# Optimization experiments

Hardware: AMD Instinct MI355X
Metric: run time of the kernel (lower is better)

The kernel has to match this reference:

```python
import jax, jax.numpy as jnp
import numpy as np

N, E, B, H, F = 20000, 400000, 200, 10, 78
HID = H * F  # 780
SEQ, VOC, EMB, NF, KS = 1000, 26, 128, 32, 8
CONV_OUT = SEQ - KS + 1  # 993


def setup_inputs() -> dict:
    key = jax.random.key(0)
    ks = jax.random.split(key, 40)
    g = lambda i, shape, s=0.05: jax.random.normal(ks[i], shape, jnp.float32) * s
    inp = {
        "x": jax.random.normal(ks[0], (N, F), jnp.float32),
        "edge_index": jax.random.randint(ks[1], (2, E), 0, N),
        "batch": jnp.sort(jax.random.randint(ks[2], (N,), 0, B)),
        "target": jax.random.randint(ks[3], (B, SEQ), 0, VOC),
        # GATConv(78 -> 78, heads=10)
        "gat_W": g(4, (F, HID)),
        "gat_a_src": g(5, (H, F)),
        "gat_a_dst": g(6, (H, F)),
        "gat_b": g(7, (HID,)),
        # GCNConv(780 -> 780)
        "gcn_W": g(8, (HID, HID)),
        "gcn_b": g(9, (HID,)),
        # graph MLP head
        "fcg1_W": g(10, (HID, 1500)), "fcg1_b": g(11, (1500,)),
        "fcg2_W": g(12, (1500, 128)), "fcg2_b": g(13, (128,)),
        # protein branch
        "emb": g(14, (VOC, EMB)),
        "cW": g(15, (NF, EMB, KS)), "cb": g(16, (NF,)),
        "fxt_W": g(17, (NF * CONV_OUT, 128)), "fxt_b": g(18, (128,)),
        # fusion MLP
        "f1_W": g(19, (256, 1024)), "f1_b": g(20, (1024,)),
        "f2_W": g(21, (1024, 512)), "f2_b": g(22, (512,)),
        "f3_W": g(23, (512, 256)), "f3_b": g(24, (256,)),
        "f4_W": g(25, (256, 128)), "f4_b": g(26, (128,)),
        "o_W": g(27, (128, 1)), "o_b": g(28, (1,)),
    }
    return inp


def _graph_branch(x, edge_index, batch, gat_W, gat_a_src, gat_a_dst, gat_b,
                  gcn_W, gcn_b, fcg1_W, fcg1_b, fcg2_W, fcg2_b):
    n = x.shape[0]
    loops = jnp.arange(n)
    src = jnp.concatenate([edge_index[0], loops])  # add self loops (PyG default)
    dst = jnp.concatenate([edge_index[1], loops])
    # --- GATConv ---
    h = (x @ gat_W).reshape(n, H, F)  # [N,H,F]
    a_s = jnp.einsum("nhf,hf->nh", h, gat_a_src)
    a_d = jnp.einsum("nhf,hf->nh", h, gat_a_dst)
    e = jax.nn.leaky_relu(a_s[src] + a_d[dst], 0.2)  # [Etot,H]
    m = jax.ops.segment_max(e, dst, num_segments=n)
    ex = jnp.exp(e - m[dst])
    den = jax.ops.segment_sum(ex, dst, num_segments=n)
    alpha = ex / den[dst]
    agg = jax.ops.segment_sum(h[src] * alpha[:, :, None], dst, num_segments=n)
    x1 = jax.nn.relu(agg.reshape(n, HID) + gat_b)
    # --- GCNConv (sym norm with self loops) ---
    deg = jax.ops.segment_sum(jnp.ones_like(dst, jnp.float32), dst, num_segments=n)
    dinv = jax.lax.rsqrt(jnp.maximum(deg, 1.0))
    norm = dinv[src] * dinv[dst]
    h2 = x1 @ gcn_W
    x2 = jax.ops.segment_sum(h2[src] * norm[:, None], dst, num_segments=n) + gcn_b
    x2 = jax.nn.relu(x2)
    # --- global add pool + MLP ---
    xg = jax.ops.segment_sum(x2, batch, num_segments=B)
    xg = jax.nn.relu(xg @ fcg1_W + fcg1_b)  # dropout = identity (eval)
    return xg @ fcg2_W + fcg2_b


def _protein_branch(target, emb, cW, cb, fxt_W, fxt_b):
    et = emb[target]  # [B,SEQ,EMB]
    c = jax.lax.conv_general_dilated(
        et.transpose(0, 2, 1), cW, (1,), "VALID",
        dimension_numbers=("NCH", "OIH", "NCH"))  # [B,NF,993]
    c = c + cb[None, :, None]
    return c.reshape(c.shape[0], NF * CONV_OUT) @ fxt_W + fxt_b


def reference(x, edge_index, batch, target, gat_W, gat_a_src, gat_a_dst, gat_b,
              gcn_W, gcn_b, fcg1_W, fcg1_b, fcg2_W, fcg2_b, emb, cW, cb,
              fxt_W, fxt_b, f1_W, f1_b, f2_W, f2_b, f3_W, f3_b, f4_W, f4_b,
              o_W, o_b):
    xg = _graph_branch(x, edge_index, batch, gat_W, gat_a_src, gat_a_dst, gat_b,
                       gcn_W, gcn_b, fcg1_W, fcg1_b, fcg2_W, fcg2_b)
    xt = _protein_branch(target, emb, cW, cb, fxt_W, fxt_b)
    xc = jnp.concatenate([xg, xt], axis=1)  # [B,256]
    xc = jax.nn.relu(xc @ f1_W + f1_b)
    xc = jax.nn.relu(xc @ f2_W + f2_b)
    xc = jax.nn.relu(xc @ f3_W + f3_b)
    xc = jax.nn.relu(xc @ f4_W + f4_b)
    return xc @ o_W + o_b  # [B,1]
```

## Files before the change

kernel.cpp:

```cpp
#include <hip/hip_runtime.h>
#include <hip/hip_bf16.h>
#include <math.h>

typedef __hip_bfloat16 bf16;
typedef __attribute__((ext_vector_type(8))) short short8v;
typedef __attribute__((ext_vector_type(4))) float float4v;

#define NODES 20000
#define EDG   400000
#define ETOT  (EDG + NODES)
#define GB    200
#define HEADS 10
#define FD    78
#define HIDD  780
#define SEQL  1000
#define VOCS  26
#define EMBD  128
#define NFC   32
#define KSZ   8
#define COUT  993
#define KFXT  (NFC * COUT)

#define MPAD  20096
#define NPADB 896
#define KP1   96
#define KP2   800
#define HP    800
#define PNL   4
#define PF    200


__device__ __forceinline__ float us2f(unsigned short u) {
  unsigned int i = ((unsigned int)u) << 16; float f; __builtin_memcpy(&f, &i, 4); return f;
}
__device__ __forceinline__ float b2f(bf16 v) { return __bfloat162float(v); }
__device__ __forceinline__ float ldany(const void* p, size_t i, int m) {
  if (m) return ((const float*)p)[i];
  return b2f(((const bf16*)p)[i]);
}
__device__ __forceinline__ bool nanf_(float v) { return v != v; }
__device__ __forceinline__ unsigned short f2us(float v) {
  bf16 b = __float2bfloat16(v); unsigned short u; __builtin_memcpy(&u, &b, 2); return u;
}

__global__ void k_detect(const void* x, int* diag) {
  int t = threadIdx.x;
  const unsigned short* u = (const unsigned short*)x;
  int hit = 0;
  for (int i = t; i < 4096; i += 256) {
    float v = us2f(u[i]);
    if (nanf_(v) || fabsf(v) > 1e6f) hit = 1;
  }
  if (hit) diag[1] = 1;
}

__global__ void k_pad_x(const void* x, bf16* xpad, const int* diag) {
  int idx = blockIdx.x * 256 + threadIdx.x;
  if (idx >= MPAD * KP1) return;
  int mode = diag[1];
  int m = idx / KP1, k = idx % KP1;
  float v = (m < NODES && k < FD) ? ldany(x, (size_t)m * FD + k, mode) : 0.f;
  xpad[idx] = __float2bfloat16(v);
}

__global__ void k_tr_gatw(const void* gw, bf16* Wt, const int* diag) {
  int idx = blockIdx.x * 256 + threadIdx.x;
  if (idx >= NPADB * KP1) return;
  int mode = diag[1];
  int n = idx / KP1, k = idx % KP1;
  float v = (n < HIDD && k < FD) ? ldany(gw, (size_t)k * HIDD + n, mode) : 0.f;
  Wt[idx] = __float2bfloat16(v);
}

__global__ void k_tr_gcnw(const void* gw, bf16* Wt, const int* diag) {
  int idx = blockIdx.x * 256 + threadIdx.x;
  if (idx >= NPADB * KP2) return;
  int mode = diag[1];
  int n = idx / KP2, k = idx % KP2;
  float v = (n < HIDD && k < HIDD) ? ldany(gw, (size_t)k * HIDD + n, mode) : 0.f;
  Wt[idx] = __float2bfloat16(v);
}

__global__ void k_zero_x1pad(bf16* x1p) {
  int i = blockIdx.x * 256 + threadIdx.x;
  if (i < (MPAD - NODES) * KP2)
    x1p[(size_t)NODES * KP2 + i] = __float2bfloat16(0.f);
}

#define MT 128
#define NT 128
#define BK 32
#define LP 40
__global__ __launch_bounds__(256) void k_gemm_mfma(const bf16* A, int lda,
                                                   const bf16* Bt, int ldb,
                                                   bf16* C, int ldc, int Ncap,
                                                   int M, int Kp) {
  __shared__ __align__(16) bf16 As[MT * LP];
  __shared__ __align__(16) bf16 Bs[NT * LP];
  int t = threadIdx.x;
  int lane = t & 63, w = t >> 6;
  int wr = (w >> 1) * 64, wc = (w & 1) * 64;
  int quad = lane >> 4, mr = lane & 15;
  int m0 = blockIdx.y * MT, n0 = blockIdx.x * NT;
  float4v acc[4][4];
#pragma unroll
  for (int i = 0; i < 4; ++i)
#pragma unroll
    for (int j = 0; j < 4; ++j) acc[i][j] = (float4v){0.f, 0.f, 0.f, 0.f};

  for (int kc = 0; kc < Kp; kc += BK) {
#pragma unroll
    for (int i = 0; i < 4; ++i) {
      int c = t + i * 256;
      int row = c >> 3, col = (c & 7) * 4;
      *(uint2*)&As[row * LP + col] =
          *(const uint2*)&A[(size_t)(m0 + row) * lda + kc + col];
      *(uint2*)&Bs[row * LP + col] =
          *(const uint2*)&Bt[(size_t)(n0 + row) * ldb + kc + col];
    }
    __syncthreads();
    short8v af[4], bfr[4];
#pragma unroll
    for (int i = 0; i < 4; ++i)
      af[i] = *(const short8v*)&As[(wr + i * 16 + mr) * LP + quad * 8];
#pragma unroll
    for (int j = 0; j < 4; ++j)
      bfr[j] = *(const short8v*)&Bs[(wc + j * 16 + mr) * LP + quad * 8];
#pragma unroll
    for (int i = 0; i < 4; ++i)
#pragma unroll
      for (int j = 0; j < 4; ++j)
        acc[i][j] = __builtin_amdgcn_mfma_f32_16x16x32_bf16(af[i], bfr[j], acc[i][j], 0, 0, 0);
    __syncthreads();
  }
#pragma unroll
  for (int i = 0; i < 4; ++i) {
    int gm0 = m0 + wr + i * 16 + quad * 4;
#pragma unroll
    for (int j = 0; j < 4; ++j) {
      int gn = n0 + wc + j * 16 + mr;
      if (gn >= Ncap) continue;
#pragma unroll
      for (int r = 0; r < 4; ++r) {
        int gm = gm0 + r;
        if (gm < M) C[(size_t)gm * ldc + gn] = __float2bfloat16(acc[i][j][r]);
      }
    }
  }
}

#define MLP_NT 64
#define MLP_BK 32
#define MLP_MT 208
#define MLP_LP 40
__global__ __launch_bounds__(256) void k_mlp_mfma(const void* A, int lda, const void* Bw,
                                                  const void* bias, float* out, int ostride,
                                                  int ooff, int M, int Nn, int K,
                                                  int ksplit, int aRelu, int aBf16,
                                                  const int* diag) {
  __shared__ __align__(16) bf16 As[MLP_MT * MLP_LP];
  __shared__ __align__(16) bf16 Bs[MLP_NT * MLP_LP];
  int mode = diag[1];
  int t = threadIdx.x;
  int lane = t & 63, w = t >> 6;
  int quad = lane >> 4, mr = lane & 15;
  int n0 = blockIdx.x * MLP_NT;
  int kz = blockIdx.y;
  int nchunks = (K + MLP_BK - 1) / MLP_BK;
  int cpk = (nchunks + ksplit - 1) / ksplit;
  int c0 = kz * cpk, c1 = c0 + cpk;
  if (c1 > nchunks) c1 = nchunks;
  float4v acc[13];
#pragma unroll
  for (int i = 0; i < 13; ++i) acc[i] = (float4v){0.f, 0.f, 0.f, 0.f};

  for (int c = c0; c < c1; ++c) {
    int k0 = c * MLP_BK;
    if (aBf16) {
      const bf16* Ab = (const bf16*)A;
      for (int e = t; e < MLP_MT * 4; e += 256) {
        int row = e >> 2, c8 = (e & 3) * 8;
        int gk = k0 + c8;
        if (row < M && gk + 7 < K) {
          *(uint4*)&As[row * MLP_LP + c8] = *(const uint4*)&Ab[(size_t)row * lda + gk];
        } else {
#pragma unroll
          for (int kk = 0; kk < 8; ++kk) {
            float v = (row < M && gk + kk < K) ? b2f(Ab[(size_t)row * lda + gk + kk]) : 0.f;
            As[row * MLP_LP + c8 + kk] = __float2bfloat16(v);
          }
        }
      }
    } else {
      const float* Af = (const float*)A;
      for (int e = t; e < MLP_MT * 8; e += 256) {
        int row = e >> 3, c4 = (e & 7) * 4;
        int gk = k0 + c4;
        float4 v4 = {0.f, 0.f, 0.f, 0.f};
        if (row < M) {
          if (gk + 3 < K) {
            v4 = *(const float4*)&Af[(size_t)row * lda + gk];
          } else {
            v4.x = (gk + 0 < K) ? Af[(size_t)row * lda + gk + 0] : 0.f;
            v4.y = (gk + 1 < K) ? Af[(size_t)row * lda + gk + 1] : 0.f;
            v4.z = (gk + 2 < K) ? Af[(size_t)row * lda + gk + 2] : 0.f;
            v4.w = (gk + 3 < K) ? Af[(size_t)row * lda + gk + 3] : 0.f;
          }
        }
        if (aRelu) {
          v4.x = fmaxf(v4.x, 0.f); v4.y = fmaxf(v4.y, 0.f);
          v4.z = fmaxf(v4.z, 0.f); v4.w = fmaxf(v4.w, 0.f);
        }
        bf16* dst = &As[row * MLP_LP + c4];
        dst[0] = __float2bfloat16(v4.x); dst[1] = __float2bfloat16(v4.y);
        dst[2] = __float2bfloat16(v4.z); dst[3] = __float2bfloat16(v4.w);
      }
    }
    for (int e = t; e < MLP_NT * MLP_BK; e += 256) {
      int k = e >> 6, col = e & 63;
      int gk = k0 + k, gn = n0 + col;
      float v = (gn < Nn && gk < K) ? ldany(Bw, (size_t)gk * Nn + gn, mode) : 0.f;
      Bs[col * MLP_LP + k] = __float2bfloat16(v);
    }
    __syncthreads();
    short8v bf = *(const short8v*)&Bs[(w * 16 + mr) * MLP_LP + quad * 8];
#pragma unroll
    for (int i = 0; i < 13; ++i) {
      short8v af = *(const short8v*)&As[(i * 16 + mr) * MLP_LP + quad * 8];
      acc[i] = __builtin_amdgcn_mfma_f32_16x16x32_bf16(af, bf, acc[i], 0, 0, 0);
    }
    __syncthreads();
  }
  int gn = n0 + w * 16 + mr;
  if (gn >= Nn) return;
  float bs = (kz == 0) ? ldany(bias, gn, mode) : 0.f;
#pragma unroll
  for (int i = 0; i < 13; ++i) {
    int gm0 = i * 16 + quad * 4;
#pragma unroll
    for (int r = 0; r < 4; ++r) {
      int gm = gm0 + r;
      if (gm >= M) break;
      float v = acc[i][r] + bs;
      float* op = &out[(size_t)gm * ostride + ooff + gn];
      if (ksplit == 1) *op = v;
      else atomicAdd(op, v);
    }
  }
}

__global__ void k_prep_ws(const void* gat_W, const void* a_src, const void* a_dst,
                          float* Ws, float* Wd, const int* diag) {
  int idx = blockIdx.x * 256 + threadIdx.x;
  if (idx >= FD * HEADS) return;
  int mode = diag[1];
  int k = idx / HEADS, hd = idx % HEADS;
  float s = 0.f, d = 0.f;
  for (int f = 0; f < FD; ++f) {
    float w = ldany(gat_W, (size_t)k * HIDD + hd * FD + f, mode);
    s += w * ldany(a_src, (size_t)hd * FD + f, mode);
    d += w * ldany(a_dst, (size_t)hd * FD + f, mode);
  }
  Ws[k * HEADS + hd] = s;
  Wd[k * HEADS + hd] = d;
}

__global__ void k_prep_mtab(const void* emb, const void* cW, float* Mtab, const int* diag) {
  int idx = blockIdx.x * 256 + threadIdx.x;
  if (idx >= NFC * KSZ * VOCS) return;
  int mode = diag[1];
  int o = idx / (KSZ * VOCS);
  int r = idx % (KSZ * VOCS);
  int k = r / VOCS, v = r % VOCS;
  float acc = 0.f;
  for (int i = 0; i < EMBD; ++i)
    acc += ldany(emb, (size_t)v * EMBD + i, mode) * ldany(cW, ((size_t)o * EMBD + i) * KSZ + k, mode);
  Mtab[idx] = acc;
}

__global__ __launch_bounds__(256) void k_asd(const void* x, const float* Ws, const float* Wd,
                                             float* a_s, float* a_d, const int* diag) {
  __shared__ unsigned short xs[256 * FD];
  __shared__ float ws_sh[FD * HEADS], wd_sh[FD * HEADS];
  int mode = diag[1];
  int nb = blockIdx.x * 256, t = threadIdx.x;
  for (int e = t; e < FD * HEADS; e += 256) { ws_sh[e] = Ws[e]; wd_sh[e] = Wd[e]; }
  for (int e = t; e < 256 * FD; e += 256) {
    int r = e / FD, c = e % FD;
    int gn = nb + r;
    float xv = (gn < NODES) ? ldany(x, (size_t)gn * FD + c, mode) : 0.f;
    xs[e] = f2us(xv);
  }
  __syncthreads();
  int n = nb + t;
  if (n >= NODES) return;
  float as[HEADS], ad[HEADS];
#pragma unroll
  for (int hd = 0; hd < HEADS; ++hd) { as[hd] = 0.f; ad[hd] = 0.f; }
  for (int f = 0; f < FD; ++f) {
    float xv = us2f(xs[t * FD + f]);
#pragma unroll
    for (int hd = 0; hd < HEADS; ++hd) {
      as[hd] += xv * ws_sh[f * HEADS + hd];
      ad[hd] += xv * wd_sh[f * HEADS + hd];
    }
  }
#pragma unroll
  for (int hd = 0; hd < HEADS; ++hd) {
    a_s[n * HEADS + hd] = as[hd];
    a_d[n * HEADS + hd] = ad[hd];
  }
}

__global__ void k_count(const int* ei, int* cnt, int* diag) {
  int e = blockIdx.x * 256 + threadIdx.x;
  if (e >= ETOT) return;
  int d = (e < EDG) ? ei[EDG + e] : (e - EDG);
  if ((unsigned)d >= NODES) { atomicOr(diag, 8192); d = 0; }
  atomicAdd(&cnt[d], 1);
}

__global__ __launch_bounds__(1024) void k_scan(const int* cnt, int* rowstart) {
  __shared__ int sh[1024];
  __shared__ int carry;
  int t = threadIdx.x;
  if (t == 0) carry = 0;
  __syncthreads();
  for (int c = 0; c < (NODES + 1023) / 1024; ++c) {
    int i = c * 1024 + t;
    int v = (i < NODES) ? cnt[i] : 0;
    sh[t] = v;
    __syncthreads();
    for (int off = 1; off < 1024; off <<= 1) {
      int add = (t >= off) ? sh[t - off] : 0;
      __syncthreads();
      sh[t] += add;
      __syncthreads();
    }
    int tot = sh[1023];
    int excl = sh[t] - v + carry;
    if (i < NODES) rowstart[i] = excl;
    __syncthreads();
    if (t == 0) carry += tot;
    __syncthreads();
  }
  if (t == 0) rowstart[NODES] = carry;
}

__global__ void k_dinv(const int* cnt, float* dinv) {
  int n = blockIdx.x * 256 + threadIdx.x;
  if (n >= NODES) return;
  int d = cnt[n];
  dinv[n] = rsqrtf((float)(d > 0 ? d : 1));
}

__global__ void k_scatter(const int* ei, const int* rowstart, int* cur, int* es_src,
                          int* diag) {
  int e = blockIdx.x * 256 + threadIdx.x;
  if (e >= ETOT) return;
  int s, d;
  if (e < EDG) { s = ei[e]; d = ei[EDG + e]; } else { s = e - EDG; d = s; }
  if ((unsigned)d >= NODES) { atomicOr(diag, 8192); d = 0; }
  if ((unsigned)s >= NODES) { atomicOr(diag, 8192); s = 0; }
  int pos = rowstart[d] + atomicAdd(&cur[d], 1);
  if ((unsigned)pos < (unsigned)ETOT) es_src[pos] = s;
  else atomicOr(diag, 1);
}

__global__ void k_csrchk(const int* cnt, const int* cur, const int* rowst, int* diag) {
  int n = blockIdx.x * 256 + threadIdx.x;
  if (n < NODES && cur[n] != cnt[n]) atomicOr(diag, 1);
  if (n == 0 && rowst[NODES] != ETOT) atomicOr(diag, 1);
}

__global__ void k_bseg(const int* batch, int* bstart, int* diag) {
  int i = blockIdx.x * 256 + threadIdx.x;
  if (i >= NODES) return;
  int bi = batch[i];
  if ((unsigned)bi >= GB) { atomicOr(diag, 8192); bi = GB - 1; }
  int bp;
  if (i == 0) bp = -1;
  else {
    bp = batch[i - 1];
    if ((unsigned)bp >= GB) bp = GB - 1;
  }
  for (int b = bp + 1; b <= bi; ++b) bstart[b] = i;
  if (i == NODES - 1)
    for (int b = bi + 1; b <= GB; ++b) bstart[b] = NODES;
}

__global__ __launch_bounds__(64) void k_alpha(const int* es_src, const int* rowst,
                                              const float* a_s, const float* a_d,
                                              float* alpha, int* diag) {
  int d = blockIdx.x, lane = threadIdx.x;
  int start = rowst[d], end = rowst[d + 1];
  float ad[HEADS];
#pragma unroll
  for (int j = 0; j < HEADS; ++j) ad[j] = a_d[d * HEADS + j];
  float mx[HEADS];
#pragma unroll
  for (int j = 0; j < HEADS; ++j) mx[j] = -INFINITY;
  for (int base = start; base < end; base += 64) {
    int ce = base + lane;
    if (ce < end) {
      int s = es_src[ce];
      if ((unsigned)s >= NODES) { atomicOr(diag, 1); s = 0; }
#pragma unroll
      for (int j = 0; j < HEADS; ++j) {
        float v = a_s[s * HEADS + j] + ad[j];
        v = v > 0.f ? v : 0.2f * v;
        mx[j] = fmaxf(mx[j], v);
      }
    }
  }
#pragma unroll
  for (int j = 0; j < HEADS; ++j)
    for (int off = 1; off < 64; off <<= 1) mx[j] = fmaxf(mx[j], __shfl_xor(mx[j], off, 64));
  float den[HEADS];
#pragma unroll
  for (int j = 0; j < HEADS; ++j) den[j] = 0.f;
  for (int base = start; base < end; base += 64) {
    int ce = base + lane;
    if (ce < end) {
      int s = es_src[ce];
      if ((unsigned)s >= NODES) s = 0;
#pragma unroll
      for (int j = 0; j < HEADS; ++j) {
        float v = a_s[s * HEADS + j] + ad[j];
        v = v > 0.f ? v : 0.2f * v;
        den[j] += expf(v - mx[j]);
      }
    }
  }
#pragma unroll
  for (int j = 0; j < HEADS; ++j)
    for (int off = 1; off < 64; off <<= 1) den[j] += __shfl_xor(den[j], off, 64);
  if (lane == 0 && (nanf_(den[0]) || nanf_(den[HEADS - 1]))) atomicOr(diag, 2);
  for (int base = start; base < end; base += 64) {
    int ce = base + lane;
    if (ce < end) {
      int s = es_src[ce];
      if ((unsigned)s >= NODES) s = 0;
#pragma unroll
      for (int j = 0; j < HEADS; ++j) {
        float v = a_s[s * HEADS + j] + ad[j];
        v = v > 0.f ? v : 0.2f * v;
        alpha[(size_t)ce * HEADS + j] = expf(v - mx[j]) / den[j];
      }
    }
  }
}

__global__ __launch_bounds__(64) void k_gatg(const int* es_src, const int* rowst,
                                             const float* alpha, const bf16* h,
                                             const void* gat_b, bf16* x1, int* diag) {
  __shared__ int ssc[64];
  __shared__ float alw[64 * HEADS];
  int bid = blockIdx.x;
  int p = bid & (PNL - 1), d = bid >> 2;
  int lane = threadIdx.x;
  int mode = diag[1];
  int start = rowst[d], end = rowst[d + 1];
  int fb = p * PF + lane * 4;
  int hA = fb / FD; if (hA > HEADS - 1) hA = HEADS - 1;
  int hB = (fb + 3) / FD; if (hB > HEADS - 1) hB = HEADS - 1;
  bool selB[4];
#pragma unroll
  for (int k = 0; k < 4; ++k) {
    int hk = (fb + k) / FD; if (hk > HEADS - 1) hk = HEADS - 1;
    selB[k] = (hk != hA);
  }
  float acc[4] = {0.f, 0.f, 0.f, 0.f};
  for (int base = start; base < end; base += 64) {
    int ce = base + lane;
    if (ce < end) {
      int s = es_src[ce];
      if ((unsigned)s >= NODES) { atomicOr(diag, 1); s = 0; }
      ssc[lane] = s;
#pragma unroll
      for (int j = 0; j < HEADS; ++j) alw[lane * HEADS + j] = alpha[(size_t)ce * HEADS + j];
    }
    __syncthreads();
    int cnt2 = end - base; if (cnt2 > 64) cnt2 = 64;
    if (lane < 50) {
      for (int e = 0; e < cnt2; ++e) {
        int ss = ssc[e];
        float aA = alw[e * HEADS + hA];
        float aB = alw[e * HEADS + hB];
        uint2 u = *(const uint2*)(h + (size_t)ss * HP + fb);
        acc[0] += (selB[0] ? aB : aA) * us2f((unsigned short)(u.x & 0xffffu));
        acc[1] += (selB[1] ? aB : aA) * us2f((unsigned short)(u.x >> 16));
        acc[2] += (selB[2] ? aB : aA) * us2f((unsigned short)(u.y & 0xffffu));
        acc[3] += (selB[3] ? aB : aA) * us2f((unsigned short)(u.y >> 16));
      }
    }
    __syncthreads();
  }
  if (lane < 50) {
    if (nanf_(acc[0]) || nanf_(acc[3])) atomicOr(diag, 8);
    unsigned short o[4];
#pragma unroll
    for (int k = 0; k < 4; ++k) {
      int f = fb + k;
      float v = 0.f;
      if (f < HIDD) v = fmaxf(acc[k] + ldany(gat_b, f, mode), 0.f);
      o[k] = f2us(v);
    }
    uint2 pack;
    __builtin_memcpy(&pack, o, 8);
    *(uint2*)(x1 + (size_t)d * KP2 + fb) = pack;
  }
}

__global__ __launch_bounds__(64) void k_gcng(const int* es_src, const int* rowst,
                                             const float* dinv, const bf16* h2,
                                             const void* gcn_b, bf16* x2b, int* diag) {
  __shared__ int ssc[64];
  __shared__ float nw[64];
  int bid = blockIdx.x;
  int p = bid & (PNL - 1), d = bid >> 2;
  int lane = threadIdx.x;
  int mode = diag[1];
  int start = rowst[d], end = rowst[d + 1];
  float dd = dinv[d];
  int fb = p * PF + lane * 4;
  float acc[4] = {0.f, 0.f, 0.f, 0.f};
  for (int base = start; base < end; base += 64) {
    int ce = base + lane;
    if (ce < end) {
      int s = es_src[ce];
      if ((unsigned)s >= NODES) { atomicOr(diag, 1); s = 0; }
      ssc[lane] = s;
      nw[lane] = dinv[s] * dd;
    }
    __syncthreads();
    int cnt2 = end - base; if (cnt2 > 64) cnt2 = 64;
    if (lane < 50) {
      for (int e = 0; e < cnt2; ++e) {
        int ss = ssc[e];
        float nv = nw[e];
        uint2 u = *(const uint2*)(h2 + (size_t)ss * HP + fb);
        acc[0] += nv * us2f((unsigned short)(u.x & 0xffffu));
        acc[1] += nv * us2f((unsigned short)(u.x >> 16));
        acc[2] += nv * us2f((unsigned short)(u.y & 0xffffu));
        acc[3] += nv * us2f((unsigned short)(u.y >> 16));
      }
    }
    __syncthreads();
  }
  if (lane < 50) {
    if (nanf_(acc[0]) || nanf_(acc[3])) atomicOr(diag, 16);
    unsigned short o[4];
#pragma unroll
    for (int k = 0; k < 4; ++k) {
      int f = fb + k;
      float v = 0.f;
      if (f < HIDD) v = fmaxf(acc[k] + ldany(gcn_b, f, mode), 0.f);
      o[k] = f2us(v);
    }
    uint2 pack;
    __builtin_memcpy(&pack, o, 8);
    *(uint2*)(x2b + (size_t)d * HP + fb) = pack;
  }
}

__global__ __launch_bounds__(256) void k_pool(const bf16* x2b, const int* bstart,
                                              float* xg_pool) {
  int b = blockIdx.x, t = threadIdx.x;
  if (t >= 195) return;
  int r0 = bstart[b], r1 = bstart[b + 1];
  int fb = t * 4;
  float4 acc = {0.f, 0.f, 0.f, 0.f};
  for (int r = r0; r < r1; ++r) {
    uint2 u = *(const uint2*)(x2b + (size_t)r * HP + fb);
    acc.x += us2f((unsigned short)(u.x & 0xffffu));
    acc.y += us2f((unsigned short)(u.x >> 16));
    acc.z += us2f((unsigned short)(u.y & 0xffffu));
    acc.w += us2f((unsigned short)(u.y >> 16));
  }
  *(float4*)&xg_pool[(size_t)b * HIDD + fb] = acc;
}

__global__ __launch_bounds__(256) void k_conv(const int* target, const float* Mtab,
                                              const void* cb, bf16* c, int* diag) {
  int b = blockIdx.y, tc = blockIdx.x, t = threadIdx.x;
  __shared__ float Mt[NFC * KSZ * VOCS];
  __shared__ int tg[256 + KSZ - 1];
  int mode = diag[1];
  for (int e = t; e < NFC * KSZ * VOCS; e += 256) Mt[e] = Mtab[e];
  int tbase = tc * 256;
  for (int e = t; e < 256 + KSZ - 1; e += 256) {
    int p = tbase + e;
    int tv = (p < SEQL) ? target[b * SEQL + p] : 0;
    if ((unsigned)tv >= VOCS) { atomicOr(diag, 8192); tv = 0; }
    tg[e] = tv;
  }
  __syncthreads();
  int tt = tbase + t;
  if (tt >= COUT) return;
  float acc[NFC];
#pragma unroll
  for (int o = 0; o < NFC; ++o) acc[o] = 0.f;
#pragma unroll
  for (int k = 0; k < KSZ; ++k) {
    int v = tg[t + k];
    const float* Mk = &Mt[k * VOCS + v];
#pragma unroll
    for (int o = 0; o < NFC; ++o) acc[o] += Mk[o * KSZ * VOCS];
  }
  if (nanf_(acc[0])) atomicOr(diag, 4096);
#pragma unroll
  for (int o = 0; o < NFC; ++o)
    c[(size_t)b * KFXT + o * COUT + tt] = __float2bfloat16(acc[o] + ldany(cb, o, mode));
}

__global__ __launch_bounds__(64) void k_out(const float* xf4, const void* o_W,
                                            const void* o_b, void* outp, const int* diag) {
  int b = blockIdx.x, lane = threadIdx.x;
  int mode = diag[1];
  float a0 = fmaxf(xf4[b * 128 + lane], 0.f);
  float a1 = fmaxf(xf4[b * 128 + 64 + lane], 0.f);
  float v = a0 * ldany(o_W, lane, mode) + a1 * ldany(o_W, 64 + lane, mode);
  for (int off = 32; off; off >>= 1) v += __shfl_down(v, off, 64);
  if (lane == 0) {
    float r = v + ldany(o_b, 0, mode);
    int dg = diag[0];
    if (dg) r = 256.f * (1 + mode) + 8.f * (float)(__ffs(dg) - 1);
    else if (nanf_(r)) r = 200.f + 100.f * mode;
    if (mode) ((float*)outp)[b] = r;
    else ((bf16*)outp)[b] = __float2bfloat16(r);
  }
}

extern "C" void kernel_launch(void* const* d_in, const int* in_sizes, int n_in,
                              void* d_out, int out_size, void* d_ws, size_t ws_size,
                              hipStream_t stream) {
  const void* x       = d_in[0];
  const int*  ei      = (const int*)d_in[1];
  const int*  batch   = (const int*)d_in[2];
  const int*  target  = (const int*)d_in[3];
  const void* gat_W   = d_in[4];
  const void* a_src   = d_in[5];
  const void* a_dst   = d_in[6];
  const void* gat_b   = d_in[7];
  const void* gcn_W   = d_in[8];
  const void* gcn_b   = d_in[9];
  const void* fcg1_W  = d_in[10];
  const void* fcg1_b  = d_in[11];
  const void* fcg2_W  = d_in[12];
  const void* fcg2_b  = d_in[13];
  const void* emb     = d_in[14];
  const void* cW      = d_in[15];
  const void* cb      = d_in[16];
  const void* fxt_W   = d_in[17];
  const void* fxt_b   = d_in[18];
  const void* f1_W    = d_in[19];
  const void* f1_b    = d_in[20];
  const void* f2_W    = d_in[21];
  const void* f2_b    = d_in[22];
  const void* f3_W    = d_in[23];
  const void* f3_b    = d_in[24];
  const void* f4_W    = d_in[25];
  const void* f4_b    = d_in[26];
  const void* o_W     = d_in[27];
  const void* o_b     = d_in[28];

  char* w = (char*)d_ws;
  size_t off = 0;
  auto alloc = [&](size_t bytes) -> void* {
    void* p = w + off;
    off = (off + bytes + 255) & ~(size_t)255;
    return p;
  };
  bf16*  h_buf   = (bf16*)alloc((size_t)NODES * HP * 2);
  bf16*  x1p     = (bf16*)alloc((size_t)MPAD * KP2 * 2);
  bf16*  xpad    = (bf16*)alloc((size_t)MPAD * KP1 * 2);
  bf16*  gatWt   = (bf16*)alloc((size_t)NPADB * KP1 * 2);
  bf16*  gcnWt   = (bf16*)alloc((size_t)NPADB * KP2 * 2);
  float* a_s     = (float*)alloc((size_t)NODES * HEADS * 4);
  float* a_d     = (float*)alloc((size_t)NODES * HEADS * 4);
  float* alpha   = (float*)alloc((size_t)ETOT * HEADS * 4);
  float* Ws      = (float*)alloc(FD * HEADS * 4);
  float* Wd      = (float*)alloc(FD * HEADS * 4);
  float* Mtab    = (float*)alloc(NFC * KSZ * VOCS * 4);
  int*   rowst   = (int*)alloc((NODES + 1) * 4);
  float* dinv    = (float*)alloc(NODES * 4);
  int*   bstart  = (int*)alloc((GB + 1) * 4);
  bf16*  c_buf   = (bf16*)alloc((size_t)GB * KFXT * 2);
  size_t zoff = off;
  int*   cnt     = (int*)alloc(NODES * 4);
  int*   cur     = (int*)alloc(NODES * 4);
  int*   es_src  = (int*)alloc((size_t)ETOT * 4);
  float* xg_pool = (float*)alloc((size_t)GB * HIDD * 4);
  float* xg1     = (float*)alloc((size_t)GB * 1500 * 4);
  float* xc      = (float*)alloc((size_t)GB * 256 * 4);
  float* xf1     = (float*)alloc((size_t)GB * 1024 * 4);
  float* xf2     = (float*)alloc((size_t)GB * 512 * 4);
  float* xf3     = (float*)alloc((size_t)GB * 256 * 4);
  float* xf4     = (float*)alloc((size_t)GB * 128 * 4);
  int*   diag    = (int*)alloc(2 * 4);
  size_t zlen = off - zoff;

  bf16* x2b = x1p;

  hipMemsetAsync(w + zoff, 0, zlen, stream);

  k_detect<<<1, 256, 0, stream>>>(x, diag);

  k_pad_x<<<(MPAD * KP1 + 255) / 256, 256, 0, stream>>>(x, xpad, diag);
  k_tr_gatw<<<(NPADB * KP1 + 255) / 256, 256, 0, stream>>>(gat_W, gatWt, diag);
  k_tr_gcnw<<<(NPADB * KP2 + 255) / 256, 256, 0, stream>>>(gcn_W, gcnWt, diag);
  k_zero_x1pad<<<((MPAD - NODES) * KP2 + 255) / 256, 256, 0, stream>>>(x1p);

  k_prep_ws<<<(FD * HEADS + 255) / 256, 256, 0, stream>>>(gat_W, a_src, a_dst, Ws, Wd, diag);
  k_prep_mtab<<<(NFC * KSZ * VOCS + 255) / 256, 256, 0, stream>>>(emb, cW, Mtab, diag);

  k_gemm_mfma<<<dim3(NPADB / NT, MPAD / MT), 256, 0, stream>>>(
      xpad, KP1, gatWt, KP1, h_buf, HP, HP, NODES, KP1);
  k_asd<<<(NODES + 255) / 256, 256, 0, stream>>>(x, Ws, Wd, a_s, a_d, diag);

  k_count<<<(ETOT + 255) / 256, 256, 0, stream>>>(ei, cnt, diag);
  k_scan<<<1, 1024, 0, stream>>>(cnt, rowst);
  k_dinv<<<(NODES + 255) / 256, 256, 0, stream>>>(cnt, dinv);
  k_scatter<<<(ETOT + 255) / 256, 256, 0, stream>>>(ei, rowst, cur, es_src, diag);
  k_csrchk<<<(NODES + 255) / 256, 256, 0, stream>>>(cnt, cur, rowst, diag);
  k_bseg<<<(NODES + 255) / 256, 256, 0, stream>>>(batch, bstart, diag);

  k_alpha<<<NODES, 64, 0, stream>>>(es_src, rowst, a_s, a_d, alpha, diag);
  k_gatg<<<NODES * PNL, 64, 0, stream>>>(es_src, rowst, alpha, h_buf, gat_b, x1p, diag);

  k_gemm_mfma<<<dim3(NPADB / NT, MPAD / MT), 256, 0, stream>>>(
      x1p, KP2, gcnWt, KP2, h_buf, HP, HP, NODES, KP2);

  k_gcng<<<NODES * PNL, 64, 0, stream>>>(es_src, rowst, dinv, h_buf, gcn_b, x2b, diag);
  k_pool<<<GB, 256, 0, stream>>>(x2b, bstart, xg_pool);

  k_conv<<<dim3(4, GB), 256, 0, stream>>>(target, Mtab, cb, c_buf, diag);

  k_mlp_mfma<<<dim3(24, 4), 256, 0, stream>>>(xg_pool, HIDD, fcg1_W, fcg1_b,
                                              xg1, 1500, 0, GB, 1500, HIDD, 4, 0, 0, diag);
  k_mlp_mfma<<<dim3(2, 16), 256, 0, stream>>>(xg1, 1500, fcg2_W, fcg2_b,
                                              xc, 256, 0, GB, 128, 1500, 16, 1, 0, diag);
  k_mlp_mfma<<<dim3(2, 64), 256, 0, stream>>>(c_buf, KFXT, fxt_W, fxt_b,
                                              xc, 256, 128, GB, 128, KFXT, 64, 0, 1, diag);
  k_mlp_mfma<<<dim3(16, 4), 256, 0, stream>>>(xc, 256, f1_W, f1_b,
                                              xf1, 1024, 0, GB, 1024, 256, 4, 0, 0, diag);
  k_mlp_mfma<<<dim3(8, 8), 256, 0, stream>>>(xf1, 1024, f2_W, f2_b,
                                             xf2, 512, 0, GB, 512, 1024, 8, 1, 0, diag);
  k_mlp_mfma<<<dim3(4, 8), 256, 0, stream>>>(xf2, 512, f3_W, f3_b,
                                             xf3, 256, 0, GB, 256, 512, 8, 1, 0, diag);
  k_mlp_mfma<<<dim3(2, 8), 256, 0, stream>>>(xf3, 256, f4_W, f4_b,
                                             xf4, 128, 0, GB, 128, 256, 8, 1, 0, diag);
  k_out<<<GB, 64, 0, stream>>>(xf4, o_W, o_b, d_out, diag);
}
```

Before: 958.6 us.

## Transpose conv output and split fxt GEMM over 128 K-slices with reduction

The protein conv now writes its output transposed ([K, batch padded to 208]), one block per filter and 32-position tile. A dedicated fxt GEMM kernel splits the 31776-long K dimension into 128 slices, writes partial sums to a scratch buffer instead of using atomics, and a separate kernel reduces them and adds the bias. The aim is more parallelism for the large-K, small-M GEMM and removal of atomic contention on xc. The cost is an extra partial buffer of 128x208x128 floats, an extra launch, and uncoalesced transposed scatter stores into the A tile in shared memory.

```diff
diff --git a/kernel.cpp b/kernel.cpp
--- a/kernel.cpp
+++ b/kernel.cpp
@@ -28,6 +28,8 @@
 #define HP    800
 #define PNL   4
 #define PF    200
+#define MB2   208
+#define FXT_KS 128
 
 
 __device__ __forceinline__ float us2f(unsigned short u) {
@@ -249,6 +251,71 @@
   }
 }
 
+__global__ __launch_bounds__(256) void k_fxt(const bf16* cT, const void* Bw,
+                                             float* part, const int* diag) {
+  __shared__ __align__(16) bf16 As[MLP_MT * MLP_LP];
+  __shared__ __align__(16) bf16 Bs[MLP_NT * MLP_LP];
+  int mode = diag[1];
+  int t = threadIdx.x;
+  int lane = t & 63, w = t >> 6;
+  int quad = lane >> 4, mr = lane & 15;
+  int n0 = blockIdx.x * MLP_NT;
+  int kz = blockIdx.y;
+  int nchunks = KFXT / MLP_BK;
+  int cpk = (nchunks + FXT_KS - 1) / FXT_KS;
+  int c0 = kz * cpk, c1 = c0 + cpk;
+  if (c1 > nchunks) c1 = nchunks;
+  float4v acc[13];
+#pragma unroll
+  for (int i = 0; i < 13; ++i) acc[i] = (float4v){0.f, 0.f, 0.f, 0.f};
+
+  for (int c = c0; c < c1; ++c) {
+    int k0 = c * MLP_BK;
+    for (int e = t; e < 32 * 52; e += 256) {
+      int kk = e / 52, bq = e % 52;
+      uint2 u = *(const uint2*)&cT[(size_t)(k0 + kk) * MB2 + bq * 4];
+      unsigned short* ap = (unsigned short*)As;
+      int mb = bq * 4;
+      ap[(mb + 0) * MLP_LP + kk] = (unsigned short)(u.x & 0xffffu);
+      ap[(mb + 1) * MLP_LP + kk] = (unsigned short)(u.x >> 16);
+      ap[(mb + 2) * MLP_LP + kk] = (unsigned short)(u.y & 0xffffu);
+      ap[(mb + 3) * MLP_LP + kk] = (unsigned short)(u.y >> 16);
+    }
+    for (int e = t; e < MLP_NT * MLP_BK; e += 256) {
+      int k = e >> 6, col = e & 63;
+      float v = ldany(Bw, (size_t)(k0 + k) * 128 + (n0 + col), mode);
+      Bs[col * MLP_LP + k] = __float2bfloat16(v);
+    }
+    __syncthreads();
+    short8v bf = *(const short8v*)&Bs[(w * 16 + mr) * MLP_LP + quad * 8];
+#pragma unroll
+    for (int i = 0; i < 13; ++i) {
+      short8v af = *(const short8v*)&As[(i * 16 + mr) * MLP_LP + quad * 8];
+      acc[i] = __builtin_amdgcn_mfma_f32_16x16x32_bf16(af, bf, acc[i], 0, 0, 0);
+    }
+    __syncthreads();
+  }
+  int gnl = n0 + w * 16 + mr;
+#pragma unroll
+  for (int i = 0; i < 13; ++i) {
+#pragma unroll
+    for (int r = 0; r < 4; ++r) {
+      int gm = i * 16 + quad * 4 + r;
+      part[((size_t)kz * MB2 + gm) * 128 + gnl] = acc[i][r];
+    }
+  }
+}
+
+__global__ __launch_bounds__(128) void k_fxt_red(const float* part, const void* bias,
+                                                 float* xc, const int* diag) {
+  int gm = blockIdx.x, n = threadIdx.x;
+  int mode = diag[1];
+  float s = 0.f;
+  for (int kz = 0; kz < FXT_KS; ++kz)
+    s += part[((size_t)kz * MB2 + gm) * 128 + n];
+  xc[(size_t)gm * 256 + 128 + n] = s + ldany(bias, n, mode);
+}
+
 __global__ void k_prep_ws(const void* gat_W, const void* a_src, const void* a_dst,
                           float* Ws, float* Wd, const int* diag) {
   int idx = blockIdx.x * 256 + threadIdx.x;
@@ -581,37 +648,37 @@
   *(float4*)&xg_pool[(size_t)b * HIDD + fb] = acc;
 }
 
-__global__ __launch_bounds__(256) void k_conv(const int* target, const float* Mtab,
-                                              const void* cb, bf16* c, int* diag) {
-  int b = blockIdx.y, tc = blockIdx.x, t = threadIdx.x;
-  __shared__ float Mt[NFC * KSZ * VOCS];
-  __shared__ int tg[256 + KSZ - 1];
-  int mode = diag[1];
-  for (int e = t; e < NFC * KSZ * VOCS; e += 256) Mt[e] = Mtab[e];
-  int tbase = tc * 256;
-  for (int e = t; e < 256 + KSZ - 1; e += 256) {
-    int p = tbase + e;
-    int tv = (p < SEQL) ? target[b * SEQL + p] : 0;
+__global__ __launch_bounds__(256) void k_convT(const int* target, const float* Mtab,
+                                               const void* cb, bf16* cT, int* diag) {
+  __shared__ int tg[GB * 40];
+  __shared__ float Mt[KSZ * VOCS];
+  int tt0 = blockIdx.x * 32, o = blockIdx.y, t = threadIdx.x;
+  int mode = diag[1];
+  for (int e = t; e < KSZ * VOCS; e += 256)
+    Mt[e] = Mtab[(o * KSZ + e / VOCS) * VOCS + (e % VOCS)];
+  for (int e = t; e < GB * 40; e += 256) {
+    int b = e / 40, q = e % 40;
+    int pos = tt0 + q;
+    int tv = (pos < SEQL) ? target[b * SEQL + pos] : 0;
     if ((unsigned)tv >= VOCS) { atomicOr(diag, 8192); tv = 0; }
     tg[e] = tv;
   }
   __syncthreads();
-  int tt = tbase + t;
-  if (tt >= COUT) return;
-  float acc[NFC];
-#pragma unroll
-  for (int o = 0; o < NFC; ++o) acc[o] = 0.f;
-#pragma unroll
-  for (int k = 0; k < KSZ; ++k) {
-    int v = tg[t + k];
-    const float* Mk = &Mt[k * VOCS + v];
-#pragma unroll
-    for (int o = 0; o < NFC; ++o) acc[o] += Mk[o * KSZ * VOCS];
-  }
-  if (nanf_(acc[0])) atomicOr(diag, 4096);
-#pragma unroll
-  for (int o = 0; o < NFC; ++o)
-    c[(size_t)b * KFXT + o * COUT + tt] = __float2bfloat16(acc[o] + ldany(cb, o, mode));
+  float cbv = ldany(cb, o, mode);
+  for (int e = t; e < 32 * MB2; e += 256) {
+    int tt = e / MB2, b = e % MB2;
+    int gtt = tt0 + tt;
+    if (gtt >= COUT) continue;
+    float acc = 0.f;
+    if (b < GB) {
+#pragma unroll
+      for (int k = 0; k < KSZ; ++k)
+        acc += Mt[k * VOCS + tg[b * 40 + tt + k]];
+      acc += cbv;
+      if (nanf_(acc)) atomicOr(diag, 4096);
+    }
+    cT[((size_t)o * COUT + gtt) * MB2 + b] = __float2bfloat16(b < GB ? acc : 0.f);
+  }
 }
 
 __global__ __launch_bounds__(64) void k_out(const float* xf4, const void* o_W,
@@ -686,7 +753,8 @@
   int*   rowst   = (int*)alloc((NODES + 1) * 4);
   float* dinv    = (float*)alloc(NODES * 4);
   int*   bstart  = (int*)alloc((GB + 1) * 4);
-  bf16*  c_buf   = (bf16*)alloc((size_t)GB * KFXT * 2);
+  bf16*  cT      = (bf16*)alloc((size_t)KFXT * MB2 * 2);
+  float* part    = (float*)alloc((size_t)FXT_KS * MB2 * 128 * 4);
   size_t zoff = off;
   int*   cnt     = (int*)alloc(NODES * 4);
   int*   cur     = (int*)alloc(NODES * 4);
@@ -735,14 +803,14 @@
   k_gcng<<<NODES * PNL, 64, 0, stream>>>(es_src, rowst, dinv, h_buf, gcn_b, x2b, diag);
   k_pool<<<GB, 256, 0, stream>>>(x2b, bstart, xg_pool);
 
-  k_conv<<<dim3(4, GB), 256, 0, stream>>>(target, Mtab, cb, c_buf, diag);
+  k_convT<<<dim3((COUT + 31) / 32, NFC), 256, 0, stream>>>(target, Mtab, cb, cT, diag);
+  k_fxt<<<dim3(2, FXT_KS), 256, 0, stream>>>(cT, fxt_W, part, diag);
+  k_fxt_red<<<GB, 128, 0, stream>>>(part, fxt_b, xc, diag);
 
   k_mlp_mfma<<<dim3(24, 4), 256, 0, stream>>>(xg_pool, HIDD, fcg1_W, fcg1_b,
                                               xg1, 1500, 0, GB, 1500, HIDD, 4, 0, 0, diag);
   k_mlp_mfma<<<dim3(2, 16), 256, 0, stream>>>(xg1, 1500, fcg2_W, fcg2_b,
                                               xc, 256, 0, GB, 128, 1500, 16, 1, 0, diag);
-  k_mlp_mfma<<<dim3(2, 64), 256, 0, stream>>>(c_buf, KFXT, fxt_W, fxt_b,
-                                              xc, 256, 128, GB, 128, KFXT, 64, 0, 1, diag);
   k_mlp_mfma<<<dim3(16, 4), 256, 0, stream>>>(xc, 256, f1_W, f1_b,
                                               xf1, 1024, 0, GB, 1024, 256, 4, 0, 0, diag);
   k_mlp_mfma<<<dim3(8, 8), 256, 0, stream>>>(xf1, 1024, f2_W, f2_b,
```

Measured after the change: 925.6 us. 3.4% less time.
